# Kernel tuning notes

Hardware: AMD Instinct MI355X
Metric: run time of the kernel (lower is better)

Reference implementation:

```python
import jax, jax.numpy as jnp
import numpy as np

D_MODEL, D_STATE, D_CONV, D_INNER = 1024, 16, 4, 2048
BATCH, SEQLEN = 4, 2048


def setup_inputs() -> dict:
    key = jax.random.key(0)
    ks = jax.random.split(key, 8)
    x = jax.random.normal(ks[0], (BATCH, SEQLEN, D_MODEL), jnp.float32)
    W_in = jax.random.normal(ks[1], (D_MODEL, 2 * D_INNER), jnp.float32) / np.float32(np.sqrt(D_MODEL))
    conv_w = jax.random.normal(ks[2], (D_INNER, 1, D_CONV), jnp.float32) * np.float32(0.3)
    W_x = jax.random.normal(ks[3], (D_INNER, 2 * D_STATE), jnp.float32) / np.float32(np.sqrt(D_INNER))
    W_dt = jax.random.normal(ks[4], (D_STATE, D_INNER), jnp.float32) / np.float32(np.sqrt(D_STATE))
    b_dt = jax.random.normal(ks[5], (D_INNER,), jnp.float32) * np.float32(0.1)
    W_Bp = jax.random.normal(ks[6], (D_STATE, D_INNER), jnp.float32) / np.float32(np.sqrt(D_STATE))
    D_param = jnp.ones((D_INNER,), jnp.float32)
    W_out = jax.random.normal(ks[7], (D_INNER, D_MODEL), jnp.float32) / np.float32(np.sqrt(D_INNER))
    return {"x": x, "W_in": W_in, "conv_w": conv_w, "W_x": W_x,
            "W_dt": W_dt, "b_dt": b_dt, "W_Bp": W_Bp, "D_param": D_param,
            "W_out": W_out}


def _mamba_fwd(x, W_in, conv_w, W_x, W_dt, b_dt, W_Bp, D_param, W_out):
    B, L, _ = x.shape
    xz = x @ W_in                                   # [B,L,2*d_inner]
    xc, z = jnp.split(xz, 2, axis=-1)
    # causal depthwise conv1d (torch pads d_conv-1 both sides then slices [:L])
    xt = jnp.transpose(xc, (0, 2, 1))               # [B,d_inner,L]
    xt = jax.lax.conv_general_dilated(
        xt, conv_w,
        window_strides=(1,), padding=[(D_CONV - 1, 0)],
        dimension_numbers=("NCH", "OIH", "NCH"),
        feature_group_count=D_INNER)
    u = jax.nn.silu(jnp.transpose(xt, (0, 2, 1)))   # [B,L,d_inner]
    xp = u @ W_x                                    # [B,L,2*d_state]
    dt_raw, B_raw = jnp.split(xp, 2, axis=-1)
    dt = jax.nn.softplus(dt_raw @ W_dt + b_dt)      # [B,L,d_inner]
    Bp = B_raw @ W_Bp                               # [B,L,d_inner]
    dt = jnp.clip(dt, 1e-4, 1.0)
    # selective scan: h_t = h_{t-1}*(1-dt_t) + u_t*Bp_t (note: A is unused in source)
    ub = u * Bp
    def step(h, inp):
        d_t, ub_t = inp
        h = h * (1.0 - d_t) + ub_t
        return h, h
    _, ys = jax.lax.scan(step, jnp.zeros((B, D_INNER), x.dtype),
                         (jnp.transpose(dt, (1, 0, 2)), jnp.transpose(ub, (1, 0, 2))))
    y = jnp.transpose(ys, (1, 0, 2)) + D_param * u  # [B,L,d_inner]
    y = y * jax.nn.silu(z)
    return y @ W_out                                # [B,L,d_model]


def reference(x, W_in, conv_w, W_x, W_dt, b_dt, W_Bp, D_param, W_out):
    # dropout is identity in eval mode
    return _mamba_fwd(x, W_in, conv_w, W_x, W_dt, b_dt, W_Bp, D_param, W_out)
```

## Files before the change

### kernel.cpp

```cpp
#include <hip/hip_runtime.h>
#include <cstdint>
#include <cstddef>

#define DM   1024
#define DI   2048
#define SEQ  2048
#define NB   4
#define NTOK (NB*SEQ)
#define CCH  32
#define LC   (SEQ/CCH)
#define KS   8

typedef __attribute__((ext_vector_type(8))) short short8v;
typedef __attribute__((ext_vector_type(4))) float f32x4;
typedef unsigned short u16;
typedef unsigned int   u32;

__device__ __forceinline__ float silu_f(float x){ return x / (1.f + __expf(-x)); }

__device__ __forceinline__ float softplus_f(float x){
  return (x > 20.f) ? x : __logf(1.f + __expf(x));
}

__device__ __forceinline__ u16 f2bf(float f){
  union { float f; u32 u; } c; c.f = f;
  u32 u = c.u + 0x7FFFu + ((c.u >> 16) & 1u);
  return (u16)(u >> 16);
}
__device__ __forceinline__ float b2f(u16 b){
  union { u32 u; float f; } c; c.u = ((u32)b) << 16; return c.f;
}
__device__ __forceinline__ float lo2f(u32 v){ union { u32 u; float f; } c; c.u = v << 16; return c.f; }
__device__ __forceinline__ float hi2f(u32 v){ union { u32 u; float f; } c; c.u = v & 0xFFFF0000u; return c.f; }
__device__ __forceinline__ u32 pack2(float a, float b){ return (u32)f2bf(a) | ((u32)f2bf(b) << 16); }

__device__ __forceinline__ void gl16(const void* g, void* l){
  __builtin_amdgcn_global_load_lds((const __attribute__((address_space(1))) void*)g,
                                   (__attribute__((address_space(3))) void*)l, 16, 0, 0);
}

__global__ __launch_bounds__(256) void cvtk(const float4* __restrict__ in,
                                            u16* __restrict__ outp, int n4)
{
  int i = blockIdx.x * 256 + threadIdx.x;
  if (i < n4) {
    float4 v = in[i];
    *(uint2*)(outp + (size_t)i * 4) = make_uint2(pack2(v.x, v.y), pack2(v.z, v.w));
  }
}

__global__ __launch_bounds__(256) void transcvt(
    const float* __restrict__ W, u16* __restrict__ Wt, int R, int Cn)
{
  __shared__ float t[64][65];
  const int tid = threadIdx.x;
  const int bx = blockIdx.x, by = blockIdx.y;
  const int lr4 = tid >> 6;
  const int lc  = tid & 63;
  #pragma unroll
  for (int p = 0; p < 16; ++p) {
    int lr = p * 4 + lr4;
    t[lr][lc] = W[(size_t)(by * 64 + lr) * Cn + bx * 64 + lc];
  }
  __syncthreads();
  #pragma unroll
  for (int p = 0; p < 16; ++p) {
    int orr = p * 4 + lr4;
    Wt[(size_t)(bx * 64 + orr) * R + by * 64 + lc] = f2bf(t[lc][orr]);
  }
}

__global__ __launch_bounds__(256) void prep_smallw(
    const float* __restrict__ W_x, const float* __restrict__ W_dt,
    const float* __restrict__ W_Bp, u16* __restrict__ Wxt, u16* __restrict__ Wbig)
{
  int i = blockIdx.x * 256 + threadIdx.x;
  if (i < 32 * DI) {
    int j = i >> 11, c = i & (DI - 1);
    Wxt[i] = f2bf(W_x[c * 32 + j]);
  }
  int i2 = i - 32 * DI;
  if (i2 >= 0 && i2 < 2 * DI * 32) {
    int n = i2 >> 5, k = i2 & 31;
    float v;
    if (n < DI) v = (k < 16) ? W_dt[k * DI + n] : 0.f;
    else        v = (k >= 16) ? W_Bp[(k - 16) * DI + (n - DI)] : 0.f;
    Wbig[i2] = f2bf(v);
  }
}

template<int NT, int OBF16>
__global__ __launch_bounds__(512, 1) void gemm3p(
    const u16* __restrict__ A, const u16* __restrict__ Bt,
    void* C0v, void* C1v, int K, int split, int ldc)
{
  __shared__ __align__(16) u16 Ab[3][128 * 64];
  __shared__ __align__(16) u16 Bb[3][256 * 64];
  const int tid = threadIdx.x, lane = tid & 63, w = tid >> 6;
  const int wm = w >> 2, wn = w & 3;
  const int bm = blockIdx.y * 128, bn = blockIdx.x * 256;

  const int lr = lane >> 3;
  const int kc = ((lane & 7) ^ lr) << 3;
  const u16* Ag = A  + (size_t)(bm + w * 8 + lr) * K + kc;
  const u16* Bg = Bt + (size_t)(bn + w * 8 + lr) * K + kc;

  const int lq = lane >> 4, l15 = lane & 15;
  const int co0 = (( lq     ) ^ (l15 & 7)) << 3;
  const int co1 = ((lq + 4) ^ (l15 & 7)) << 3;
  const int abase = (wm * 64 + l15) * 64;
  const int bbase = (wn * 64 + l15) * 64;

  f32x4 acc[4][4] = {};

  auto issue = [&](int t, int buf) {
    const size_t k0 = (size_t)t << 6;
    #pragma unroll
    for (int q = 0; q < 2; ++q)
      gl16(Ag + (size_t)q * 64 * K + k0, &Ab[buf][q * 4096 + w * 512]);
    #pragma unroll
    for (int q = 0; q < 4; ++q)
      gl16(Bg + (size_t)q * 64 * K + k0, &Bb[buf][q * 4096 + w * 512]);
  };
  auto compute = [&](int buf) {
    const u16* Ac = Ab[buf];
    const u16* Bc = Bb[buf];
    short8v af[4], bf[4];
    #pragma unroll
    for (int ks = 0; ks < 2; ++ks) {
      const int co = ks ? co1 : co0;
      #pragma unroll
      for (int i = 0; i < 4; ++i) af[i] = *(const short8v*)&Ac[abase + i * 1024 + co];
      #pragma unroll
      for (int j = 0; j < 4; ++j) bf[j] = *(const short8v*)&Bc[bbase + j * 1024 + co];
      __builtin_amdgcn_s_setprio(1);
      #pragma unroll
      for (int i = 0; i < 4; ++i)
        #pragma unroll
        for (int j = 0; j < 4; ++j)
          acc[i][j] = __builtin_amdgcn_mfma_f32_16x16x32_bf16(af[i], bf[j], acc[i][j], 0, 0, 0);
      __builtin_amdgcn_s_setprio(0);
    }
  };

  issue(0, 0); issue(1, 1); issue(2, 2);
  int cur = 0;
  #pragma unroll 1
  for (int t = 0; t < NT - 2; ++t) {
    asm volatile("s_waitcnt vmcnt(12)" ::: "memory");
    __builtin_amdgcn_s_barrier(); __builtin_amdgcn_sched_barrier(0);
    compute(cur);
    __builtin_amdgcn_s_barrier(); __builtin_amdgcn_sched_barrier(0);
    if (t + 3 < NT) issue(t + 3, cur);
    cur = (cur == 2) ? 0 : cur + 1;
  }
  asm volatile("s_waitcnt vmcnt(6)" ::: "memory");
  __builtin_amdgcn_s_barrier(); __builtin_amdgcn_sched_barrier(0);
  compute(cur);
  cur = (cur == 2) ? 0 : cur + 1;
  asm volatile("s_waitcnt vmcnt(0)" ::: "memory");
  __builtin_amdgcn_s_barrier(); __builtin_amdgcn_sched_barrier(0);
  compute(cur);

  const bool left = (bn < split);
  const int cb = bn - (left ? 0 : split) + wn * 64 + l15;
  const int rb = bm + wm * 64 + lq * 4;
  if (OBF16) {
    u16* Cp = (u16*)(left ? C0v : C1v);
    #pragma unroll
    for (int i = 0; i < 4; ++i)
      #pragma unroll
      for (int j = 0; j < 4; ++j)
        #pragma unroll
        for (int r = 0; r < 4; ++r)
          Cp[(size_t)(rb + i * 16 + r) * ldc + cb + j * 16] = f2bf(acc[i][j][r]);
  } else {
    float* Cp = (float*)(left ? C0v : C1v);
    #pragma unroll
    for (int i = 0; i < 4; ++i)
      #pragma unroll
      for (int j = 0; j < 4; ++j)
        #pragma unroll
        for (int r = 0; r < 4; ++r)
          Cp[(size_t)(rb + i * 16 + r) * ldc + cb + j * 16] = acc[i][j][r];
  }
}

__global__ __launch_bounds__(256) void xp_gemm(
    const u16* __restrict__ A, const u16* __restrict__ Bt, float* __restrict__ xpp)
{
  __shared__ __align__(16) u16 Asm[128 * 32];
  __shared__ __align__(16) u16 Bsm[32 * 32];
  const int tid = threadIdx.x, lane = tid & 63, w = tid >> 6;
  const int bm = blockIdx.x * 128;
  const int kbase = blockIdx.y * (DI / KS);
  f32x4 acc[2][2] = {};
  const int srow = w * 32 + (lane >> 2);
  const int soct = lane & 3;
  const u16* Ap = A + (size_t)(bm + srow) * DI + kbase + soct * 8;
  const u16* Bp = Bt + (size_t)(lane >> 2) * DI + kbase + soct * 8;
  u16* As0 = &Asm[w * 1024];

  for (int k0 = 0; k0 < DI / KS; k0 += 32) {
    gl16(Ap + k0,                      As0);
    gl16(Ap + k0 + (size_t)16 * DI,    As0 + 512);
    if (w == 0) {
      gl16(Bp + k0,                    Bsm);
      gl16(Bp + k0 + (size_t)16 * DI,  Bsm + 512);
    }
    __syncthreads();
    short8v af[2], bf[2];
    #pragma unroll
    for (int i = 0; i < 2; ++i)
      af[i] = *(const short8v*)&Asm[(w * 32 + i * 16 + (lane & 15)) * 32 + (lane >> 4) * 8];
    #pragma unroll
    for (int j = 0; j < 2; ++j)
      bf[j] = *(const short8v*)&Bsm[(j * 16 + (lane & 15)) * 32 + (lane >> 4) * 8];
    #pragma unroll
    for (int i = 0; i < 2; ++i)
      #pragma unroll
      for (int j = 0; j < 2; ++j)
        acc[i][j] = __builtin_amdgcn_mfma_f32_16x16x32_bf16(af[i], bf[j], acc[i][j], 0, 0, 0);
    __syncthreads();
  }
  float* op = xpp + (size_t)blockIdx.y * NTOK * 32;
  const int rb = bm + w * 32 + (lane >> 4) * 4;
  const int cb = lane & 15;
  #pragma unroll
  for (int i = 0; i < 2; ++i)
    #pragma unroll
    for (int j = 0; j < 2; ++j)
      #pragma unroll
      for (int r = 0; r < 4; ++r)
        op[(size_t)(rb + i * 16 + r) * 32 + cb + j * 16] = acc[i][j][r];
}

__global__ __launch_bounds__(256) void xp_reduce(
    const float* __restrict__ xpp, u16* __restrict__ xpb)
{
  int i = blockIdx.x * 256 + threadIdx.x;
  float s = 0.f;
  #pragma unroll
  for (int k = 0; k < KS; ++k) s += xpp[(size_t)k * NTOK * 32 + i];
  xpb[i] = f2bf(s);
}

__global__ __launch_bounds__(256) void dtub_gemm(
    const u16* __restrict__ A, const u16* __restrict__ Bt,
    const float* __restrict__ b_dt, const u16* __restrict__ u,
    u16* __restrict__ dt_out, u16* __restrict__ ub_out)
{
  __shared__ __align__(16) u16 Asm[128 * 32];
  __shared__ __align__(16) u16 Bsm[128 * 32];
  const int tid = threadIdx.x, lane = tid & 63, w = tid >> 6;
  const int wm = w >> 1, wn = w & 1;
  const int bm = blockIdx.y * 128, bn = blockIdx.x * 128;
  const int srow = w * 32 + (lane >> 2);
  const int soct = lane & 3;
  u16* As0 = &Asm[w * 1024];
  u16* Bs0 = &Bsm[w * 1024];
  gl16(A  + (size_t)(bm + srow) * 32 + soct * 8,       As0);
  gl16(A  + (size_t)(bm + srow) * 32 + soct * 8 + 512, As0 + 512);
  gl16(Bt + (size_t)(bn + srow) * 32 + soct * 8,       Bs0);
  gl16(Bt + (size_t)(bn + srow) * 32 + soct * 8 + 512, Bs0 + 512);
  __syncthreads();
  f32x4 acc[4][4] = {};
  short8v afr[4], bfr[4];
  #pragma unroll
  for (int i = 0; i < 4; ++i) {
    afr[i] = *(const short8v*)&Asm[(wm * 64 + i * 16 + (lane & 15)) * 32 + (lane >> 4) * 8];
    bfr[i] = *(const short8v*)&Bsm[(wn * 64 + i * 16 + (lane & 15)) * 32 + (lane >> 4) * 8];
  }
  #pragma unroll
  for (int i = 0; i < 4; ++i)
    #pragma unroll
    for (int j = 0; j < 4; ++j)
      acc[i][j] = __builtin_amdgcn_mfma_f32_16x16x32_bf16(afr[i], bfr[j], acc[i][j], 0, 0, 0);

  const int rb = bm + wm * 64 + (lane >> 4) * 4;
  const int cb = bn + wn * 64 + (lane & 15);
  if (bn < DI) {
    float bd[4];
    #pragma unroll
    for (int j = 0; j < 4; ++j) bd[j] = b_dt[cb + j * 16];
    #pragma unroll
    for (int i = 0; i < 4; ++i)
      #pragma unroll
      for (int j = 0; j < 4; ++j)
        #pragma unroll
        for (int r = 0; r < 4; ++r) {
          float sp = softplus_f(acc[i][j][r] + bd[j]);
          sp = fminf(fmaxf(sp, 1e-4f), 1.0f);
          dt_out[(size_t)(rb + i * 16 + r) * DI + cb + j * 16] = f2bf(sp);
        }
  } else {
    const int cn = cb - DI;
    #pragma unroll
    for (int i = 0; i < 4; ++i)
      #pragma unroll
      for (int j = 0; j < 4; ++j)
        #pragma unroll
        for (int r = 0; r < 4; ++r) {
          size_t off = (size_t)(rb + i * 16 + r) * DI + cn + j * 16;
          ub_out[off] = f2bf(b2f(u[off]) * acc[i][j][r]);
        }
  }
}

__global__ __launch_bounds__(256) void conv_silu_k(
    const u16* __restrict__ xc, const float* __restrict__ cw, u16* __restrict__ u)
{
  int idx = blockIdx.x * 256 + threadIdx.x;
  int c = (idx & (DI / 2 - 1)) << 1;
  int r = idx >> 10;
  int t = r & (SEQ - 1);
  float4 w0 = ((const float4*)cw)[c];
  float4 w1 = ((const float4*)cw)[c + 1];
  const u16* base = xc + (size_t)r * DI + c;
  u32 v = *(const u32*)base;
  float a0 = w0.w * lo2f(v), a1 = w1.w * hi2f(v);
  if (t >= 1) { v = *(const u32*)(base - DI);     a0 += w0.z * lo2f(v); a1 += w1.z * hi2f(v); }
  if (t >= 2) { v = *(const u32*)(base - 2 * DI); a0 += w0.y * lo2f(v); a1 += w1.y * hi2f(v); }
  if (t >= 3) { v = *(const u32*)(base - 3 * DI); a0 += w0.x * lo2f(v); a1 += w1.x * hi2f(v); }
  *(u32*)(u + (size_t)r * DI + c) = pack2(silu_f(a0), silu_f(a1));
}

__global__ __launch_bounds__(256) void scan_p1(
    const u16* __restrict__ dt_, const u16* __restrict__ ub,
    float* __restrict__ P, float* __restrict__ S)
{
  int idx = blockIdx.x * 256 + threadIdx.x;
  int di = (idx & (DI / 2 - 1)) << 1;
  int bc = idx >> 10;
  int c  = bc & (CCH - 1);
  int b  = bc >> 5;
  size_t base = ((size_t)b * SEQ + (size_t)c * LC) * DI + di;
  float p0 = 1.f, s0 = 0.f, p1 = 1.f, s1 = 0.f;
  #pragma unroll 4
  for (int t = 0; t < LC; ++t) {
    size_t off = base + (size_t)t * DI;
    u32 dv = *(const u32*)(dt_ + off);
    u32 uv = *(const u32*)(ub + off);
    float a0 = 1.f - lo2f(dv), a1 = 1.f - hi2f(dv);
    s0 = s0 * a0 + lo2f(uv); p0 *= a0;
    s1 = s1 * a1 + hi2f(uv); p1 *= a1;
  }
  ((float2*)P)[idx] = make_float2(p0, p1);
  ((float2*)S)[idx] = make_float2(s0, s1);
}

__global__ __launch_bounds__(256) void scan_p2(
    const float* __restrict__ P, const float* __restrict__ S, float* __restrict__ Hin)
{
  int idx = blockIdx.x * 256 + threadIdx.x;
  int di = idx & (DI - 1);
  int b  = idx >> 11;
  float h = 0.f;
  #pragma unroll
  for (int c = 0; c < CCH; ++c) {
    size_t off = ((size_t)b * CCH + c) * DI + di;
    Hin[off] = h;
    h = h * P[off] + S[off];
  }
}

__global__ __launch_bounds__(256) void scan_p3(
    const u16* dt_, const u16* __restrict__ ub, const u16* __restrict__ u,
    const u16* __restrict__ z, const float* __restrict__ Dp_,
    const float* __restrict__ Hin, u16* y)
{
  int idx = blockIdx.x * 256 + threadIdx.x;
  int di = (idx & (DI / 2 - 1)) << 1;
  int bc = idx >> 10;
  int c  = bc & (CCH - 1);
  int b  = bc >> 5;
  float2 dp = ((const float2*)Dp_)[di >> 1];
  float2 h2 = ((const float2*)Hin)[idx];
  float h0 = h2.x, h1 = h2.y;
  size_t base = ((size_t)b * SEQ + (size_t)c * LC) * DI + di;
  #pragma unroll 4
  for (int t = 0; t < LC; ++t) {
    size_t off = base + (size_t)t * DI;
    u32 dv = *(const u32*)(dt_ + off);
    u32 uv = *(const u32*)(ub + off);
    u32 uu = *(const u32*)(u + off);
    u32 zv = *(const u32*)(z + off);
    h0 = h0 * (1.f - lo2f(dv)) + lo2f(uv);
    h1 = h1 * (1.f - hi2f(dv)) + hi2f(uv);
    float y0 = (h0 + dp.x * lo2f(uu)) * silu_f(lo2f(zv));
    float y1 = (h1 + dp.y * hi2f(uu)) * silu_f(hi2f(zv));
    *(u32*)(y + off) = pack2(y0, y1);
  }
}

extern "C" void kernel_launch(void* const* d_in, const int* in_sizes, int n_in,
                              void* d_out, int out_size, void* d_ws, size_t ws_size,
                              hipStream_t stream)
{
  const float* x     = (const float*)d_in[0];
  const float* W_in  = (const float*)d_in[1];
  const float* cw    = (const float*)d_in[2];
  const float* W_x   = (const float*)d_in[3];
  const float* W_dt  = (const float*)d_in[4];
  const float* b_dt  = (const float*)d_in[5];
  const float* W_Bp  = (const float*)d_in[6];
  const float* Dp    = (const float*)d_in[7];
  const float* W_out = (const float*)d_in[8];
  float* out = (float*)d_out;

  const size_t SZ = (size_t)NTOK * DI;
  float* w    = (float*)d_ws;
  float* bufA = w;
  float* bufB = w + SZ;
  float* bufC = w + 2 * SZ;
  float* bufD = w + 3 * SZ;

  u16* xcb  = (u16*)bufA;
  u16* zb   = (u16*)bufB;
  u16* wtob = zb + (size_t)NTOK * DI;
  u16* wxt  = wtob + (size_t)DM * DI;
  u16* wbig = wxt + (size_t)32 * DI;
  u16* xbf  = (u16*)bufC;
  u16* wtib = xbf + (size_t)NTOK * DM;
  u16* ubf  = (u16*)bufC;
  u16* ubb  = (u16*)bufD;

  const size_t PS = (size_t)NB * CCH * DI;
  float* Pbuf   = out;
  float* Sbuf   = out + PS;
  float* Hin    = out + 2 * PS;
  float* xppart = out + 3 * PS;
  u16*   xpb    = (u16*)(out + 3 * PS + (size_t)KS * NTOK * 32);
  (void)ws_size; (void)in_sizes; (void)n_in; (void)out_size;

  cvtk<<<(NTOK * DM / 4) / 256, 256, 0, stream>>>((const float4*)x, xbf, NTOK * DM / 4);
  transcvt<<<dim3((2 * DI) / 64, DM / 64), 256, 0, stream>>>(W_in, wtib, DM, 2 * DI);
  transcvt<<<dim3(DM / 64, DI / 64), 256, 0, stream>>>(W_out, wtob, DI, DM);
  prep_smallw<<<(32 * DI + 2 * DI * 32) / 256, 256, 0, stream>>>(W_x, W_dt, W_Bp, wxt, wbig);

  gemm3p<DM / 64, 1><<<dim3((2 * DI) / 256, NTOK / 128), 512, 0, stream>>>(
      xbf, wtib, (void*)xcb, (void*)zb, DM, DI, DI);

  conv_silu_k<<<(NTOK * DI / 2) / 256, 256, 0, stream>>>(xcb, cw, ubf);

  xp_gemm<<<dim3(NTOK / 128, KS), 256, 0, stream>>>(ubf, wxt, xppart);
  xp_reduce<<<(NTOK * 32) / 256, 256, 0, stream>>>(xppart, xpb);
  dtub_gemm<<<dim3((2 * DI) / 128, NTOK / 128), 256, 0, stream>>>(
      xpb, wbig, b_dt, ubf, xcb, ubb);

  scan_p1<<<(NB * CCH * DI / 2) / 256, 256, 0, stream>>>(xcb, ubb, Pbuf, Sbuf);
  scan_p2<<<(NB * DI) / 256, 256, 0, stream>>>(Pbuf, Sbuf, Hin);
  scan_p3<<<(NB * CCH * DI / 2) / 256, 256, 0, stream>>>(xcb, ubb, ubf, zb, Dp, Hin, xcb);

  gemm3p<DI / 64, 0><<<dim3(DM / 256, NTOK / 128), 512, 0, stream>>>(
      xcb, wtob, (void*)out, (void*)out, DI, DM, DM);
}
```

Baseline: 328.1 us.

## Replace 128x256 triple-buffered GEMM with 128x128 double-buffered two-blocks-per-CU GEMM

The two large bf16 GEMMs move from a 512-thread, 128x256-tile, three-stage LDS pipeline to a 256-thread, 128x128-tile, two-stage pipeline with launch bounds allowing two blocks per CU. The load mapping and wait counts are reworked to match. The aim is more resident blocks and more grid parallelism so that blocks hide each other's memory latency. In exchange each tile reuses its operands less and has a shallower prefetch depth, which raises global and LDS traffic per FLOP.

```diff
diff --git a/kernel.cpp b/kernel.cpp
--- a/kernel.cpp
+++ b/kernel.cpp
@@ -90,23 +90,23 @@
 }
 
 template<int NT, int OBF16>
-__global__ __launch_bounds__(512, 1) void gemm3p(
+__global__ __launch_bounds__(256, 2) void gemm2b(
     const u16* __restrict__ A, const u16* __restrict__ Bt,
     void* C0v, void* C1v, int K, int split, int ldc)
 {
-  __shared__ __align__(16) u16 Ab[3][128 * 64];
-  __shared__ __align__(16) u16 Bb[3][256 * 64];
+  __shared__ __align__(16) u16 Ab[2][128 * 64];
+  __shared__ __align__(16) u16 Bb[2][128 * 64];
   const int tid = threadIdx.x, lane = tid & 63, w = tid >> 6;
-  const int wm = w >> 2, wn = w & 3;
-  const int bm = blockIdx.y * 128, bn = blockIdx.x * 256;
-
-  const int lr = lane >> 3;
-  const int kc = ((lane & 7) ^ lr) << 3;
-  const u16* Ag = A  + (size_t)(bm + w * 8 + lr) * K + kc;
-  const u16* Bg = Bt + (size_t)(bn + w * 8 + lr) * K + kc;
+  const int wm = w >> 1, wn = w & 1;
+  const int bm = blockIdx.y * 128, bn = blockIdx.x * 128;
+
+  const int srow8 = tid >> 3;
+  const int kc = ((tid & 7) ^ (srow8 & 7)) << 3;
+  const u16* Ag = A  + (size_t)(bm + srow8) * K + kc;
+  const u16* Bg = Bt + (size_t)(bn + srow8) * K + kc;
 
   const int lq = lane >> 4, l15 = lane & 15;
-  const int co0 = (( lq     ) ^ (l15 & 7)) << 3;
+  const int co0 = ((lq    ) ^ (l15 & 7)) << 3;
   const int co1 = ((lq + 4) ^ (l15 & 7)) << 3;
   const int abase = (wm * 64 + l15) * 64;
   const int bbase = (wn * 64 + l15) * 64;
@@ -116,11 +116,11 @@
   auto issue = [&](int t, int buf) {
     const size_t k0 = (size_t)t << 6;
     #pragma unroll
-    for (int q = 0; q < 2; ++q)
-      gl16(Ag + (size_t)q * 64 * K + k0, &Ab[buf][q * 4096 + w * 512]);
-    #pragma unroll
     for (int q = 0; q < 4; ++q)
-      gl16(Bg + (size_t)q * 64 * K + k0, &Bb[buf][q * 4096 + w * 512]);
+      gl16(Ag + (size_t)(q * 32) * K + k0, &Ab[buf][q * 2048 + tid * 8]);
+    #pragma unroll
+    for (int q = 0; q < 4; ++q)
+      gl16(Bg + (size_t)(q * 32) * K + k0, &Bb[buf][q * 2048 + tid * 8]);
   };
   auto compute = [&](int buf) {
     const u16* Ac = Ab[buf];
@@ -143,24 +143,16 @@
     }
   };
 
-  issue(0, 0); issue(1, 1); issue(2, 2);
-  int cur = 0;
+  issue(0, 0); issue(1, 1);
   #pragma unroll 1
-  for (int t = 0; t < NT - 2; ++t) {
-    asm volatile("s_waitcnt vmcnt(12)" ::: "memory");
+  for (int t = 0; t < NT; ++t) {
+    if (t + 1 < NT) asm volatile("s_waitcnt vmcnt(8)" ::: "memory");
+    else            asm volatile("s_waitcnt vmcnt(0)" ::: "memory");
     __builtin_amdgcn_s_barrier(); __builtin_amdgcn_sched_barrier(0);
-    compute(cur);
+    compute(t & 1);
     __builtin_amdgcn_s_barrier(); __builtin_amdgcn_sched_barrier(0);
-    if (t + 3 < NT) issue(t + 3, cur);
-    cur = (cur == 2) ? 0 : cur + 1;
-  }
-  asm volatile("s_waitcnt vmcnt(6)" ::: "memory");
-  __builtin_amdgcn_s_barrier(); __builtin_amdgcn_sched_barrier(0);
-  compute(cur);
-  cur = (cur == 2) ? 0 : cur + 1;
-  asm volatile("s_waitcnt vmcnt(0)" ::: "memory");
-  __builtin_amdgcn_s_barrier(); __builtin_amdgcn_sched_barrier(0);
-  compute(cur);
+    if (t + 2 < NT) issue(t + 2, t & 1);
+  }
 
   const bool left = (bn < split);
   const int cb = bn - (left ? 0 : split) + wn * 64 + l15;
@@ -438,7 +430,7 @@
   transcvt<<<dim3(DM / 64, DI / 64), 256, 0, stream>>>(W_out, wtob, DI, DM);
   prep_smallw<<<(32 * DI + 2 * DI * 32) / 256, 256, 0, stream>>>(W_x, W_dt, W_Bp, wxt, wbig);
 
-  gemm3p<DM / 64, 1><<<dim3((2 * DI) / 256, NTOK / 128), 512, 0, stream>>>(
+  gemm2b<DM / 64, 1><<<dim3((2 * DI) / 128, NTOK / 128), 256, 0, stream>>>(
       xbf, wtib, (void*)xcb, (void*)zb, DM, DI, DI);
 
   conv_silu_k<<<(NTOK * DI / 2) / 256, 256, 0, stream>>>(xcb, cw, ubf);
@@ -452,6 +444,6 @@
   scan_p2<<<(NB * DI) / 256, 256, 0, stream>>>(Pbuf, Sbuf, Hin);
   scan_p3<<<(NB * CCH * DI / 2) / 256, 256, 0, stream>>>(xcb, ubb, ubf, zb, Dp, Hin, xcb);
 
-  gemm3p<DI / 64, 0><<<dim3(DM / 256, NTOK / 128), 512, 0, stream>>>(
+  gemm2b<DI / 64, 0><<<dim3(DM / 128, NTOK / 128), 256, 0, stream>>>(
       xcb, wtob, (void*)out, (void*)out, DI, DM, DM);
 }
```

New measurement: 299.9 us. -8.6%, faster.
